# Kernel tuning notes

Hardware: AMD Instinct MI355X
Metric: run time of the kernel (lower is better)

## Reference

```python
import jax, jax.numpy as jnp
import numpy as np

K = 20  # n_neighbors

def _edge_features(x, k):
    # x: [B, C, N] -> edge features [B, 2C, N, k] using dynamic kNN graph
    sq = jnp.sum(x * x, axis=1)                          # [B, N]
    inner = jnp.einsum('bcn,bcm->bnm', x, x)             # [B, N, N]
    neg_dist = 2.0 * inner - sq[:, :, None] - sq[:, None, :]
    idx = jax.lax.top_k(neg_dist, k)[1]                  # [B, N, k] nearest neighbors
    # gather neighbor features: xj[b,c,n,j] = x[b,c,idx[b,n,j]]
    xj = jnp.take_along_axis(x[:, :, None, :], idx[:, None, :, :], axis=3)  # [B, C, N, k]
    xi = jnp.broadcast_to(x[:, :, :, None], xj.shape)
    return jnp.concatenate([xj - xi, xi], axis=1)        # [B, 2C, N, k]

def _lrelu(v):
    return jax.nn.leaky_relu(v, 0.2)

def _edge_conv(x, W, b, k):
    f = _edge_features(x, k)                              # [B, 2C, N, k]
    h = jnp.einsum('bcnk,oc->bonk', f, W) + b[None, :, None, None]
    return jnp.max(_lrelu(h), axis=3)                     # [B, O, N]

def setup_inputs() -> dict:
    key = jax.random.key(0)
    ks = jax.random.split(key, 12)
    conv_dims = (64, 64, 128, 256)
    in_dims = (3, 64, 64, 128)
    inp = {'x': jax.random.normal(ks[0], (16, 2048, 3), dtype=jnp.float32)}
    for i, (ci, co) in enumerate(zip(in_dims, conv_dims)):
        s = 1.0 / np.sqrt(2 * ci)
        inp[f'W{i}'] = jax.random.uniform(ks[1 + 2 * i], (co, 2 * ci), jnp.float32, -s, s)
        inp[f'b{i}'] = jax.random.uniform(ks[2 + 2 * i], (co,), jnp.float32, -s, s)
    sf = 1.0 / np.sqrt(sum(conv_dims))
    inp['Wf'] = jax.random.uniform(ks[9], (1024, sum(conv_dims)), jnp.float32, -sf, sf)
    inp['bf'] = jax.random.uniform(ks[10], (1024,), jnp.float32, -sf, sf)
    return inp

def reference(x, W0, b0, W1, b1, W2, b2, W3, b3, Wf, bf):
    h = jnp.transpose(x, (0, 2, 1))                       # [B, 3, N]
    xs = []
    for W, b in ((W0, b0), (W1, b1), (W2, b2), (W3, b3)):
        h = _edge_conv(h, W, b, K)
        xs.append(h)
    h = jnp.concatenate(xs, axis=1)                       # [B, 512, N]
    h = _lrelu(jnp.einsum('bcn,oc->bon', h, Wf) + bf[None, :, None])  # [B, 1024, N]
    return jnp.max(h, axis=2)                             # [B, 1024]
```

## Files before the change

### kernel.cpp

```cpp
#include <hip/hip_runtime.h>
#include <hip/hip_bf16.h>
#include <math.h>

#define NPTS 2048
#define NB 16
#define KNN 20

typedef __attribute__((ext_vector_type(8))) short bf16x8;
typedef __attribute__((ext_vector_type(4))) float f32x4;

__device__ __forceinline__ float lrelu(float v) { return fmaxf(v, 0.2f * v); }

__device__ __forceinline__ void split2(float a, float b, unsigned& hp, unsigned& lp) {
    float2 f2; f2.x = a; f2.y = b;
    __hip_bfloat162 h2 = __float22bfloat162_rn(f2);
    unsigned hb; __builtin_memcpy(&hb, &h2, 4);
    float la = a - __uint_as_float(hb << 16);
    float lb = b - __uint_as_float(hb & 0xFFFF0000u);
    float2 l2; l2.x = la; l2.y = lb;
    __hip_bfloat162 k2 = __float22bfloat162_rn(l2);
    unsigned lb2; __builtin_memcpy(&lb2, &k2, 4);
    hp = hb; lp = lb2;
}

template<int CTRL, int RM>
__device__ __forceinline__ float dpp_fmax_step(float x) {
    int t = __builtin_amdgcn_update_dpp((int)0xFF800000, __float_as_int(x),
                                        CTRL, RM, 0xF, false);
    return fmaxf(x, __int_as_float(t));
}
__device__ __forceinline__ float wave_max_bcast(float x) {
    x = dpp_fmax_step<0x111, 0xF>(x);
    x = dpp_fmax_step<0x112, 0xF>(x);
    x = dpp_fmax_step<0x114, 0xF>(x);
    x = dpp_fmax_step<0x118, 0xF>(x);
    x = dpp_fmax_step<0x142, 0xA>(x);
    x = dpp_fmax_step<0x143, 0xC>(x);
    return __int_as_float(__builtin_amdgcn_readlane(__float_as_int(x), 63));
}

__global__ void transpose_kernel(const float* __restrict__ x, float* __restrict__ h0) {
    int t = blockIdx.x * blockDim.x + threadIdx.x;
    if (t >= NB * NPTS) return;
    int b = t / NPTS, n = t % NPTS;
    const float* src = x + (size_t)t * 3;
    float* dst = h0 + (size_t)b * 3 * NPTS + n;
    dst[0]        = src[0];
    dst[NPTS]     = src[1];
    dst[2 * NPTS] = src[2];
}

__global__ void sq_kernel(const float* __restrict__ in, long bstride, int C,
                          float* __restrict__ sq) {
    int t = blockIdx.x * blockDim.x + threadIdx.x;
    if (t >= NB * NPTS) return;
    int b = t / NPTS, n = t % NPTS;
    const float* p = in + (size_t)b * bstride + n;
    float s = 0.f;
    for (int c = 0; c < C; ++c) {
        float v = p[(size_t)c * NPTS];
        s = fmaf(v, v, s);
    }
    sq[t] = s;
}

template<int C>
__global__ __launch_bounds__(256) void knn_kernel(const float* __restrict__ xin, long bstride,
                                                  const float* __restrict__ sq,
                                                  int* __restrict__ idx) {
    __shared__ __align__(16) float xi4[C][4];
    __shared__ __align__(16) float dist[4][NPTS];
    int b = blockIdx.y;
    int n0 = blockIdx.x * 4;
    int tid = threadIdx.x;
    const float* xb = xin + (size_t)b * bstride;

    for (int e = tid; e < 4 * C; e += 256) {
        int r = e & 3, c = e >> 2;
        xi4[c][r] = xb[(size_t)c * NPTS + n0 + r];
    }
    __syncthreads();

    float acc[4][2][4];
#pragma unroll
    for (int r = 0; r < 4; ++r)
#pragma unroll
        for (int uu = 0; uu < 2; ++uu)
#pragma unroll
            for (int e = 0; e < 4; ++e) acc[r][uu][e] = 0.f;

#pragma unroll 4
    for (int c = 0; c < C; ++c) {
        float4 wv = *reinterpret_cast<const float4*>(&xi4[c][0]);
        const float* row = xb + (size_t)c * NPTS;
#pragma unroll
        for (int uu = 0; uu < 2; ++uu) {
            float4 xv = *reinterpret_cast<const float4*>(&row[4 * tid + 1024 * uu]);
            acc[0][uu][0] = fmaf(wv.x, xv.x, acc[0][uu][0]);
            acc[0][uu][1] = fmaf(wv.x, xv.y, acc[0][uu][1]);
            acc[0][uu][2] = fmaf(wv.x, xv.z, acc[0][uu][2]);
            acc[0][uu][3] = fmaf(wv.x, xv.w, acc[0][uu][3]);
            acc[1][uu][0] = fmaf(wv.y, xv.x, acc[1][uu][0]);
            acc[1][uu][1] = fmaf(wv.y, xv.y, acc[1][uu][1]);
            acc[1][uu][2] = fmaf(wv.y, xv.z, acc[1][uu][2]);
            acc[1][uu][3] = fmaf(wv.y, xv.w, acc[1][uu][3]);
            acc[2][uu][0] = fmaf(wv.z, xv.x, acc[2][uu][0]);
            acc[2][uu][1] = fmaf(wv.z, xv.y, acc[2][uu][1]);
            acc[2][uu][2] = fmaf(wv.z, xv.z, acc[2][uu][2]);
            acc[2][uu][3] = fmaf(wv.z, xv.w, acc[2][uu][3]);
            acc[3][uu][0] = fmaf(wv.w, xv.x, acc[3][uu][0]);
            acc[3][uu][1] = fmaf(wv.w, xv.y, acc[3][uu][1]);
            acc[3][uu][2] = fmaf(wv.w, xv.z, acc[3][uu][2]);
            acc[3][uu][3] = fmaf(wv.w, xv.w, acc[3][uu][3]);
        }
    }
    {
        const float* sqb = sq + (size_t)b * NPTS;
#pragma unroll
        for (int uu = 0; uu < 2; ++uu) {
            int m = 4 * tid + 1024 * uu;
            float4 sv = *reinterpret_cast<const float4*>(&sqb[m]);
            int p = m ^ (((m >> 5) & 7) << 2);
#pragma unroll
            for (int r = 0; r < 4; ++r) {
                float4 dv;
                dv.x = 2.f * acc[r][uu][0] - sv.x;
                dv.y = 2.f * acc[r][uu][1] - sv.y;
                dv.z = 2.f * acc[r][uu][2] - sv.z;
                dv.w = 2.f * acc[r][uu][3] - sv.w;
                *reinterpret_cast<float4*>(&dist[r][p]) = dv;
            }
        }
    }
    __syncthreads();

    int w = tid >> 6;
    int lane = tid & 63;
    float v[32];
    {
        const float* drow = &dist[w][32 * lane];
        int s = (lane & 7) << 2;
#pragma unroll
        for (int u = 0; u < 8; ++u) {
            float4 t = *reinterpret_cast<const float4*>(&drow[(4 * u) ^ s]);
            v[4 * u + 0] = t.x; v[4 * u + 1] = t.y;
            v[4 * u + 2] = t.z; v[4 * u + 3] = t.w;
        }
    }

    float gm[4]; int gi[4];
#pragma unroll
    for (int g = 0; g < 4; ++g) {
        gm[g] = v[8 * g]; gi[g] = 8 * g;
#pragma unroll
        for (int i = 1; i < 8; ++i)
            if (v[8 * g + i] > gm[g]) { gm[g] = v[8 * g + i]; gi[g] = 8 * g + i; }
    }
    float lv = gm[0]; int lm = gi[0];
#pragma unroll
    for (int g = 1; g < 4; ++g) if (gm[g] > lv) { lv = gm[g]; lm = gi[g]; }

    int rbm = 0;
    int* out = idx + ((size_t)b * NPTS + n0 + w) * KNN;

    for (int j = 0; j < KNN; ++j) {
        float gv = wave_max_bcast(lv);
        unsigned long long mk = __ballot(lv == gv);
        int winner = (int)__builtin_ctzll(mk);
        int wm = __builtin_amdgcn_readlane(lm, winner);
        int bm = winner * 32 + wm;
        rbm = (lane == j) ? bm : rbm;

        bool iswin = (lane == winner);
        int g = wm >> 3, ii = wm & 7;
#pragma unroll
        for (int gq = 0; gq < 4; ++gq) {
            if (gq == g) {
#pragma unroll
                for (int i = 0; i < 8; ++i)
                    v[8 * gq + i] = (iswin && (ii == i)) ? -INFINITY : v[8 * gq + i];
                float nm = v[8 * gq]; int ni = 8 * gq;
#pragma unroll
                for (int i = 1; i < 8; ++i)
                    if (v[8 * gq + i] > nm) { nm = v[8 * gq + i]; ni = 8 * gq + i; }
                gm[gq] = iswin ? nm : gm[gq];
                gi[gq] = iswin ? ni : gi[gq];
            }
        }
        lv = gm[0]; lm = gi[0];
#pragma unroll
        for (int g2 = 1; g2 < 4; ++g2) if (gm[g2] > lv) { lv = gm[g2]; lm = gi[g2]; }
    }
    if (lane < KNN) out[lane] = rbm;
}

__global__ void prep_w_kernel(const float* __restrict__ W, int C, int O,
                              float* __restrict__ Wa, float* __restrict__ Wd) {
    int t = blockIdx.x * blockDim.x + threadIdx.x;
    if (t >= C * O) return;
    int c = t / O, o = t % O;
    float a = W[o * 2 * C + c];
    float d = W[o * 2 * C + C + c] - a;
    Wa[c * O + o] = a;
    Wd[c * O + o] = d;
}

__global__ __launch_bounds__(256) void edge_mm_kernel(const float* __restrict__ xin, long bstride,
                                                      int C, int O,
                                                      const float* __restrict__ Wa,
                                                      const float* __restrict__ Wd,
                                                      const float* __restrict__ bias,
                                                      float* __restrict__ y,
                                                      float* __restrict__ base, long base_bstride) {
    int m = blockIdx.x * 256 + threadIdx.x;
    int ngrp = O >> 3;
    int og = blockIdx.y % ngrp, b = blockIdx.y / ngrp;
    int o0 = og * 8;
    const float* xb = xin + (size_t)b * bstride + m;
    float a1[8], a2[8];
#pragma unroll
    for (int i = 0; i < 8; ++i) { a1[i] = 0.f; a2[i] = 0.f; }
#pragma unroll 2
    for (int c = 0; c < C; ++c) {
        float h = xb[(size_t)c * NPTS];
        const float* wa = Wa + c * O + o0;
        const float* wd = Wd + c * O + o0;
#pragma unroll
        for (int i = 0; i < 8; ++i) {
            a1[i] = fmaf(wa[i], h, a1[i]);
            a2[i] = fmaf(wd[i], h, a2[i]);
        }
    }
#pragma unroll
    for (int i = 0; i < 8; ++i) {
        y[((size_t)b * O + o0 + i) * NPTS + m] = a1[i];
        base[(size_t)b * base_bstride + (size_t)(o0 + i) * NPTS + m] = a2[i] + bias[o0 + i];
    }
}

__global__ __launch_bounds__(256) void gather_max_kernel(const float* __restrict__ y, int O,
                                                         const int* __restrict__ idx,
                                                         float* __restrict__ feat_slice,
                                                         long bstride) {
    __shared__ float yrow[NPTS];
    int o = blockIdx.x, b = blockIdx.y;
    const float* ysrc = y + ((size_t)b * O + o) * NPTS;
    for (int m = threadIdx.x; m < NPTS; m += 256) yrow[m] = ysrc[m];
    __syncthreads();
    float* fs = feat_slice + (size_t)b * bstride + (size_t)o * NPTS;
    const int* ib = idx + (size_t)b * NPTS * KNN;
    for (int s = 0; s < 8; ++s) {
        int n = threadIdx.x + 256 * s;
        const int* ip = ib + n * KNN;
        float mx = -INFINITY;
#pragma unroll
        for (int j = 0; j < KNN; ++j) mx = fmaxf(mx, yrow[ip[j]]);
        fs[n] = lrelu(mx + fs[n]);
    }
}

__global__ void wf_split_kernel(const float* __restrict__ Wf,
                                unsigned* __restrict__ Wfh, unsigned* __restrict__ Wfl) {
    int t = blockIdx.x * 256 + threadIdx.x;
    if (t >= 262144) return;
    unsigned h, l;
    split2(Wf[2 * t], Wf[2 * t + 1], h, l);
    Wfh[t] = h; Wfl[t] = l;
}

#define GP 40
__global__ __launch_bounds__(256) void final_gemm_mfma(
    const float* __restrict__ feat,
    const unsigned short* __restrict__ Wfh,
    const unsigned short* __restrict__ Wfl,
    float* __restrict__ pmax) {
    __shared__ __align__(16) unsigned short Ah[128 * GP];
    __shared__ __align__(16) unsigned short Al[128 * GP];
    __shared__ __align__(16) unsigned short Bh[128 * GP];
    __shared__ __align__(16) unsigned short Bl[128 * GP];

    int ot = blockIdx.x, nt = blockIdx.y, b = blockIdx.z;
    int o0 = ot * 128, n0 = nt * 128;
    int tid = threadIdx.x;
    int lane = tid & 63, w = tid >> 6;
    int wm = w & 1, wn = w >> 1;
    int l15 = lane & 15, q = lane >> 4;

    f32x4 acc[4][4];
#pragma unroll
    for (int mi = 0; mi < 4; ++mi)
#pragma unroll
        for (int ni = 0; ni < 4; ++ni) acc[mi][ni] = (f32x4)0.f;

    const float* fb = feat + (size_t)b * 512 * NPTS;

    int bn = tid & 127, kh = tid >> 7;

    for (int c0 = 0; c0 < 512; c0 += 32) {
#pragma unroll
        for (int p = 0; p < 2; ++p) {
            int e = p * 256 + tid;
            int r = e >> 2, qq = e & 3;
            size_t go = (size_t)(o0 + r) * 512 + c0 + qq * 8;
            *(uint4*)&Ah[r * GP + qq * 8] = *(const uint4*)(Wfh + go);
            *(uint4*)&Al[r * GP + qq * 8] = *(const uint4*)(Wfl + go);
        }
        {
            const float* src = fb + (size_t)(c0 + kh * 16) * NPTS + n0 + bn;
            float v[16];
#pragma unroll
            for (int j = 0; j < 16; ++j) v[j] = src[(size_t)j * NPTS];
            unsigned hw[8], lw[8];
#pragma unroll
            for (int p = 0; p < 8; ++p) split2(v[2 * p], v[2 * p + 1], hw[p], lw[p]);
            unsigned short* bh = &Bh[bn * GP + kh * 16];
            unsigned short* bl = &Bl[bn * GP + kh * 16];
            *(uint4*)(bh)     = make_uint4(hw[0], hw[1], hw[2], hw[3]);
            *(uint4*)(bh + 8) = make_uint4(hw[4], hw[5], hw[6], hw[7]);
            *(uint4*)(bl)     = make_uint4(lw[0], lw[1], lw[2], lw[3]);
            *(uint4*)(bl + 8) = make_uint4(lw[4], lw[5], lw[6], lw[7]);
        }
        __syncthreads();

        bf16x8 bhf[4], blf[4];
#pragma unroll
        for (int ni = 0; ni < 4; ++ni) {
            int row = wn * 64 + ni * 16 + l15;
            bhf[ni] = *(const bf16x8*)&Bh[row * GP + q * 8];
            blf[ni] = *(const bf16x8*)&Bl[row * GP + q * 8];
        }
#pragma unroll
        for (int mi = 0; mi < 4; ++mi) {
            int row = wm * 64 + mi * 16 + l15;
            bf16x8 ah = *(const bf16x8*)&Ah[row * GP + q * 8];
            bf16x8 al = *(const bf16x8*)&Al[row * GP + q * 8];
#pragma unroll
            for (int ni = 0; ni < 4; ++ni) {
                acc[mi][ni] = __builtin_amdgcn_mfma_f32_16x16x32_bf16(ah, bhf[ni], acc[mi][ni], 0, 0, 0);
                acc[mi][ni] = __builtin_amdgcn_mfma_f32_16x16x32_bf16(ah, blf[ni], acc[mi][ni], 0, 0, 0);
                acc[mi][ni] = __builtin_amdgcn_mfma_f32_16x16x32_bf16(al, bhf[ni], acc[mi][ni], 0, 0, 0);
            }
        }
        __syncthreads();
    }

    int slot = nt * 2 + wn;
#pragma unroll
    for (int mi = 0; mi < 4; ++mi) {
        float m4[4];
#pragma unroll
        for (int r = 0; r < 4; ++r) {
            float m = acc[mi][0][r];
            m = fmaxf(m, acc[mi][1][r]);
            m = fmaxf(m, acc[mi][2][r]);
            m = fmaxf(m, acc[mi][3][r]);
            m4[r] = m;
        }
#pragma unroll
        for (int off = 1; off < 16; off <<= 1) {
#pragma unroll
            for (int r = 0; r < 4; ++r)
                m4[r] = fmaxf(m4[r], __shfl_xor(m4[r], off, 16));
        }
        if (l15 == 0) {
            int mbase = o0 + wm * 64 + mi * 16 + q * 4;
#pragma unroll
            for (int r = 0; r < 4; ++r)
                pmax[((size_t)b * 1024 + mbase + r) * 32 + slot] = m4[r];
        }
    }
}

__global__ void final_reduce_kernel(const float* __restrict__ pmax,
                                    const float* __restrict__ bf,
                                    float* __restrict__ out) {
    int t = blockIdx.x * blockDim.x + threadIdx.x;
    if (t >= NB * 1024) return;
    const float* p = pmax + (size_t)t * 32;
    float m = p[0];
#pragma unroll
    for (int i = 1; i < 32; ++i) m = fmaxf(m, p[i]);
    out[t] = lrelu(m + bf[t & 1023]);
}

extern "C" void kernel_launch(void* const* d_in, const int* in_sizes, int n_in,
                              void* d_out, int out_size, void* d_ws, size_t ws_size,
                              hipStream_t stream) {
    const float* x  = (const float*)d_in[0];
    const float* W[4]  = {(const float*)d_in[1], (const float*)d_in[3],
                          (const float*)d_in[5], (const float*)d_in[7]};
    const float* bb[4] = {(const float*)d_in[2], (const float*)d_in[4],
                          (const float*)d_in[6], (const float*)d_in[8]};
    const float* Wf = (const float*)d_in[9];
    const float* bf = (const float*)d_in[10];
    float* out = (float*)d_out;

    float* ws   = (float*)d_ws;
    float* h0   = ws;
    float* sq   = h0 + 98304;
    int*   idx  = (int*)(sq + 32768);
    float* y    = (float*)(idx + 655360);
    float* feat = y + 8388608;
    float* Wa   = feat + 16777216 + 262144;
    float* Wd   = Wa + 32768;

    unsigned* Wfh = (unsigned*)y;
    unsigned* Wfl = (unsigned*)(y + 262144);
    float*    pmax = y + 524288;

    transpose_kernel<<<128, 256, 0, stream>>>(x, h0);

    const int  Cs[4]   = {3, 64, 64, 128};
    const int  Os[4]   = {64, 64, 128, 256};
    const int  offs[4] = {0, 64, 128, 256};

    for (int l = 0; l < 4; ++l) {
        const float* in = (l == 0) ? h0 : feat + (size_t)offs[l - 1] * NPTS;
        long bstr = (l == 0) ? (long)3 * NPTS : (long)512 * NPTS;
        int C = Cs[l], O = Os[l];

        sq_kernel<<<128, 256, 0, stream>>>(in, bstr, C, sq);

        dim3 kg(NPTS / 4, NB);
        if (C == 3)       knn_kernel<3>  <<<kg, 256, 0, stream>>>(in, bstr, sq, idx);
        else if (C == 64) knn_kernel<64> <<<kg, 256, 0, stream>>>(in, bstr, sq, idx);
        else              knn_kernel<128><<<kg, 256, 0, stream>>>(in, bstr, sq, idx);

        prep_w_kernel<<<(C * O + 255) / 256, 256, 0, stream>>>(W[l], C, O, Wa, Wd);

        float* fslice = feat + (size_t)offs[l] * NPTS;
        edge_mm_kernel<<<dim3(NPTS / 256, NB * (O >> 3)), 256, 0, stream>>>(
            in, bstr, C, O, Wa, Wd, bb[l], y, fslice, (long)512 * NPTS);

        gather_max_kernel<<<dim3(O, NB), 256, 0, stream>>>(y, O, idx, fslice, (long)512 * NPTS);
    }

    wf_split_kernel<<<1024, 256, 0, stream>>>(Wf, Wfh, Wfl);
    final_gemm_mfma<<<dim3(8, 16, NB), 256, 0, stream>>>(
        feat, (const unsigned short*)Wfh, (const unsigned short*)Wfl, pmax);
    final_reduce_kernel<<<64, 256, 0, stream>>>(pmax, bf, out);
}
```

Measured before the change: 1.304 ms.

## Fuse squared-norm computation into kNN kernel and process eight query rows per block

Drops the separate sq_kernel. Each kNN thread now accumulates the squared norms of its own four candidate columns while it computes the inner products. Each block now handles 8 query points with 512 threads, each thread covering 4 columns, instead of 4 points with 256 threads, and query values are read straight from global memory rather than staged in LDS. This removes one launch per layer and halves the number of times each candidate column is re-read across blocks. In exchange it uses twice the dist LDS per block and more accumulator registers, which may reduce occupancy.

Measured after the change: 1.154 ms. -11.5%, faster.

```diff
diff --git a/kernel.cpp b/kernel.cpp
--- a/kernel.cpp
+++ b/kernel.cpp
@@ -50,86 +50,51 @@
     dst[2 * NPTS] = src[2];
 }
 
-__global__ void sq_kernel(const float* __restrict__ in, long bstride, int C,
-                          float* __restrict__ sq) {
-    int t = blockIdx.x * blockDim.x + threadIdx.x;
-    if (t >= NB * NPTS) return;
-    int b = t / NPTS, n = t % NPTS;
-    const float* p = in + (size_t)b * bstride + n;
-    float s = 0.f;
-    for (int c = 0; c < C; ++c) {
-        float v = p[(size_t)c * NPTS];
-        s = fmaf(v, v, s);
-    }
-    sq[t] = s;
-}
-
 template<int C>
-__global__ __launch_bounds__(256) void knn_kernel(const float* __restrict__ xin, long bstride,
-                                                  const float* __restrict__ sq,
+__global__ __launch_bounds__(512) void knn_kernel(const float* __restrict__ xin, long bstride,
                                                   int* __restrict__ idx) {
-    __shared__ __align__(16) float xi4[C][4];
-    __shared__ __align__(16) float dist[4][NPTS];
+    __shared__ __align__(16) float dist[8][NPTS];
     int b = blockIdx.y;
-    int n0 = blockIdx.x * 4;
+    int n0 = blockIdx.x * 8;
     int tid = threadIdx.x;
     const float* xb = xin + (size_t)b * bstride;
-
-    for (int e = tid; e < 4 * C; e += 256) {
-        int r = e & 3, c = e >> 2;
-        xi4[c][r] = xb[(size_t)c * NPTS + n0 + r];
-    }
-    __syncthreads();
-
-    float acc[4][2][4];
-#pragma unroll
-    for (int r = 0; r < 4; ++r)
-#pragma unroll
-        for (int uu = 0; uu < 2; ++uu)
-#pragma unroll
-            for (int e = 0; e < 4; ++e) acc[r][uu][e] = 0.f;
+    const float* xq = xb + n0;
+
+    int m0 = 4 * tid;
+    float4 acc[8];
+#pragma unroll
+    for (int r = 0; r < 8; ++r) acc[r] = make_float4(0.f, 0.f, 0.f, 0.f);
+    float4 sn = make_float4(0.f, 0.f, 0.f, 0.f);
 
 #pragma unroll 4
     for (int c = 0; c < C; ++c) {
-        float4 wv = *reinterpret_cast<const float4*>(&xi4[c][0]);
-        const float* row = xb + (size_t)c * NPTS;
-#pragma unroll
-        for (int uu = 0; uu < 2; ++uu) {
-            float4 xv = *reinterpret_cast<const float4*>(&row[4 * tid + 1024 * uu]);
-            acc[0][uu][0] = fmaf(wv.x, xv.x, acc[0][uu][0]);
-            acc[0][uu][1] = fmaf(wv.x, xv.y, acc[0][uu][1]);
-            acc[0][uu][2] = fmaf(wv.x, xv.z, acc[0][uu][2]);
-            acc[0][uu][3] = fmaf(wv.x, xv.w, acc[0][uu][3]);
-            acc[1][uu][0] = fmaf(wv.y, xv.x, acc[1][uu][0]);
-            acc[1][uu][1] = fmaf(wv.y, xv.y, acc[1][uu][1]);
-            acc[1][uu][2] = fmaf(wv.y, xv.z, acc[1][uu][2]);
-            acc[1][uu][3] = fmaf(wv.y, xv.w, acc[1][uu][3]);
-            acc[2][uu][0] = fmaf(wv.z, xv.x, acc[2][uu][0]);
-            acc[2][uu][1] = fmaf(wv.z, xv.y, acc[2][uu][1]);
-            acc[2][uu][2] = fmaf(wv.z, xv.z, acc[2][uu][2]);
-            acc[2][uu][3] = fmaf(wv.z, xv.w, acc[2][uu][3]);
-            acc[3][uu][0] = fmaf(wv.w, xv.x, acc[3][uu][0]);
-            acc[3][uu][1] = fmaf(wv.w, xv.y, acc[3][uu][1]);
-            acc[3][uu][2] = fmaf(wv.w, xv.z, acc[3][uu][2]);
-            acc[3][uu][3] = fmaf(wv.w, xv.w, acc[3][uu][3]);
+        const float* rowc = xb + (size_t)c * NPTS;
+        float4 xv = *reinterpret_cast<const float4*>(&rowc[m0]);
+        float4 q0 = *reinterpret_cast<const float4*>(&xq[(size_t)c * NPTS]);
+        float4 q1 = *reinterpret_cast<const float4*>(&xq[(size_t)c * NPTS + 4]);
+        sn.x = fmaf(xv.x, xv.x, sn.x);
+        sn.y = fmaf(xv.y, xv.y, sn.y);
+        sn.z = fmaf(xv.z, xv.z, sn.z);
+        sn.w = fmaf(xv.w, xv.w, sn.w);
+        float q[8] = {q0.x, q0.y, q0.z, q0.w, q1.x, q1.y, q1.z, q1.w};
+#pragma unroll
+        for (int r = 0; r < 8; ++r) {
+            acc[r].x = fmaf(q[r], xv.x, acc[r].x);
+            acc[r].y = fmaf(q[r], xv.y, acc[r].y);
+            acc[r].z = fmaf(q[r], xv.z, acc[r].z);
+            acc[r].w = fmaf(q[r], xv.w, acc[r].w);
         }
     }
     {
-        const float* sqb = sq + (size_t)b * NPTS;
-#pragma unroll
-        for (int uu = 0; uu < 2; ++uu) {
-            int m = 4 * tid + 1024 * uu;
-            float4 sv = *reinterpret_cast<const float4*>(&sqb[m]);
-            int p = m ^ (((m >> 5) & 7) << 2);
-#pragma unroll
-            for (int r = 0; r < 4; ++r) {
-                float4 dv;
-                dv.x = 2.f * acc[r][uu][0] - sv.x;
-                dv.y = 2.f * acc[r][uu][1] - sv.y;
-                dv.z = 2.f * acc[r][uu][2] - sv.z;
-                dv.w = 2.f * acc[r][uu][3] - sv.w;
-                *reinterpret_cast<float4*>(&dist[r][p]) = dv;
-            }
+        int p = m0 ^ (((m0 >> 5) & 7) << 2);
+#pragma unroll
+        for (int r = 0; r < 8; ++r) {
+            float4 dv;
+            dv.x = 2.f * acc[r].x - sn.x;
+            dv.y = 2.f * acc[r].y - sn.y;
+            dv.z = 2.f * acc[r].z - sn.z;
+            dv.w = 2.f * acc[r].w - sn.w;
+            *reinterpret_cast<float4*>(&dist[r][p]) = dv;
         }
     }
     __syncthreads();
@@ -397,8 +362,7 @@
 
     float* ws   = (float*)d_ws;
     float* h0   = ws;
-    float* sq   = h0 + 98304;
-    int*   idx  = (int*)(sq + 32768);
+    int*   idx  = (int*)(ws + 98304 + 32768);
     float* y    = (float*)(idx + 655360);
     float* feat = y + 8388608;
     float* Wa   = feat + 16777216 + 262144;
@@ -419,12 +383,10 @@
         long bstr = (l == 0) ? (long)3 * NPTS : (long)512 * NPTS;
         int C = Cs[l], O = Os[l];
 
-        sq_kernel<<<128, 256, 0, stream>>>(in, bstr, C, sq);
-
-        dim3 kg(NPTS / 4, NB);
-        if (C == 3)       knn_kernel<3>  <<<kg, 256, 0, stream>>>(in, bstr, sq, idx);
-        else if (C == 64) knn_kernel<64> <<<kg, 256, 0, stream>>>(in, bstr, sq, idx);
-        else              knn_kernel<128><<<kg, 256, 0, stream>>>(in, bstr, sq, idx);
+        dim3 kg(NPTS / 8, NB);
+        if (C == 3)       knn_kernel<3>  <<<kg, 512, 0, stream>>>(in, bstr, idx);
+        else if (C == 64) knn_kernel<64> <<<kg, 512, 0, stream>>>(in, bstr, idx);
+        else              knn_kernel<128><<<kg, 512, 0, stream>>>(in, bstr, idx);
 
         prep_w_kernel<<<(C * O + 255) / 256, 256, 0, stream>>>(W[l], C, O, Wa, Wd);
 
```
